# Kernel optimization log

Hardware: AMD Instinct MI355X
Metric: run time of the kernel (lower is better)

Reference implementation:

```python
import jax, jax.numpy as jnp
import numpy as np

NUM_MAX_PATHS = 10
LANE_FEAT_DIM = 128
SEQ_LEN = 80
BATCH = 256

def setup_inputs() -> dict:
    key = jax.random.key(0)
    ks = jax.random.split(key, 8)
    H = LANE_FEAT_DIM
    return {
        "agent_past_motion_context": jax.random.normal(ks[0], (BATCH, 128), dtype=jnp.float32),
        "possible_lanes": jax.random.normal(ks[1], (SEQ_LEN, BATCH * NUM_MAX_PATHS, 2), dtype=jnp.float32),
        "W_emb": jax.random.normal(ks[2], (H, 5), dtype=jnp.float32) * 0.1,
        "b_emb": jax.random.normal(ks[3], (H,), dtype=jnp.float32) * 0.1,
        "W_ih": jax.random.normal(ks[4], (4 * H, H), dtype=jnp.float32) * 0.1,
        "W_hh": jax.random.normal(ks[5], (4 * H, H), dtype=jnp.float32) * 0.1,
        "b_ih": jax.random.normal(ks[6], (4 * H,), dtype=jnp.float32) * 0.1,
        "b_hh": jax.random.normal(ks[7], (4 * H,), dtype=jnp.float32) * 0.1,
    }

def _lane_features(lanes):
    # lanes: [S, BL, 2]. Build 5-dim feature: (x, y, dx, dy, yaw).
    diff = lanes[1:] - lanes[:-1]                        # [S-1, BL, 2]
    diff = jnp.concatenate([jnp.zeros_like(lanes[:1]), diff], axis=0)
    # yaw = atan2(y, x) vs reference vector (1, 0)
    yaw = jnp.arctan2(lanes[..., 1], lanes[..., 0])      # [S, BL]
    ext = jnp.concatenate([lanes, diff, yaw[..., None]], axis=-1)  # [S, BL, 5]
    # lanes containing any NaN produce all-zero features (original conditional)
    valid = jnp.logical_not(jnp.any(jnp.isnan(lanes), axis=(0, 2)))  # [BL]
    return jnp.where(valid[None, :, None], ext, 0.0)

def _lstm(emb, W_ih, W_hh, b_ih, b_hh):
    H = W_hh.shape[1]
    BL = emb.shape[1]
    # precompute input projections for all steps: [S, BL, 4H]
    x_proj = jnp.einsum('sbi,gi->sbg', emb, W_ih) + b_ih

    def step(carry, xg):
        h, c = carry
        gates = xg + h @ W_hh.T + b_hh
        i, f, g, o = jnp.split(gates, 4, axis=-1)
        c = jax.nn.sigmoid(f) * c + jax.nn.sigmoid(i) * jnp.tanh(g)
        h = jax.nn.sigmoid(o) * jnp.tanh(c)
        return (h, c), None

    h0 = jnp.zeros((BL, H), dtype=emb.dtype)
    (h, c), _ = jax.lax.scan(step, (h0, h0), x_proj)
    return h

def reference(agent_past_motion_context, possible_lanes, W_emb, b_emb, W_ih, W_hh, b_ih, b_hh):
    b = agent_past_motion_context.shape[0]
    BL = possible_lanes.shape[1]
    num_max_paths = BL // b
    H = W_emb.shape[0]
    ext = _lane_features(possible_lanes)                         # [S, BL, 5]
    emb = jax.nn.relu(ext @ W_emb.T + b_emb)                     # [S, BL, H]
    h = _lstm(emb, W_ih, W_hh, b_ih, b_hh)                       # [BL, H]
    return h.reshape(b, num_max_paths, H)
```

## Files before the change

kernel.cpp:

```cpp
#include <hip/hip_runtime.h>
#include <stdint.h>

#define S_LEN 80
#define H_DIM 128
#define ROWS 10
#define MROWS 16
#define BLOCK_T 512

#define NL2E  (-1.44269504088896f)
#define N2L2E (-2.88539008177793f)

typedef __bf16 bf16x8 __attribute__((ext_vector_type(8)));
typedef unsigned short u16x8 __attribute__((ext_vector_type(8)));
typedef unsigned short u16x4 __attribute__((ext_vector_type(4)));
typedef float f32x4 __attribute__((ext_vector_type(4)));

__device__ __forceinline__ float sigy(float y) {
    return __builtin_amdgcn_rcpf(1.0f + __builtin_amdgcn_exp2f(y));
}
__device__ __forceinline__ float tanhy(float y) {
    return 2.0f * __builtin_amdgcn_rcpf(1.0f + __builtin_amdgcn_exp2f(y)) - 1.0f;
}
__device__ __forceinline__ unsigned short bfbits(float f) {
    return __builtin_bit_cast(unsigned short, (__bf16)f);
}

#define MFMA16(acc, va, wb) \
    asm("v_mfma_f32_16x16x32_bf16 %0, %1, %2, %0" : "+v"(acc) : "v"(va), "a"(wb))

__global__ __launch_bounds__(BLOCK_T, 2)
void lane_lstm(const float* __restrict__ lanes,
               const float* __restrict__ W_emb, const float* __restrict__ b_emb,
               const float* __restrict__ W_ih,  const float* __restrict__ W_hh,
               const float* __restrict__ b_ih,  const float* __restrict__ b_hh,
               float* __restrict__ out, int BL)
{
    __shared__ __align__(16) float ext_lds[S_LEN * ROWS * 5];
    __shared__ __align__(16) unsigned short emb_lds[2][MROWS * H_DIM];
    __shared__ __align__(16) unsigned short h_lds[2][MROWS * H_DIM];
    __shared__ int valid_lds[MROWS];

    const int t    = threadIdx.x;
    const int lane = t & 63;
    const int wv   = t >> 6;
    const int row0 = blockIdx.x * ROWS;

    if (t < MROWS) valid_lds[t] = 1;
    {
        u16x4 z = {0, 0, 0, 0};
        *(u16x4*)((char*)&h_lds[0][0] + t * 8) = z;
    }
    __syncthreads();

    for (int p = t; p < S_LEN * ROWS; p += BLOCK_T) {
        int s = p / ROWS;
        int r = p - s * ROWS;
        int bl = row0 + r;
        float x = 0.f, y = 0.f, dx = 0.f, dy = 0.f;
        if (bl < BL) {
            const float* lp = lanes + ((size_t)s * BL + bl) * 2;
            x = lp[0]; y = lp[1];
            if (s > 0) {
                const float* lq = lanes + ((size_t)(s - 1) * BL + bl) * 2;
                dx = x - lq[0]; dy = y - lq[1];
            }
            if (__builtin_isnan(x) || __builtin_isnan(y)) valid_lds[r] = 0;
        }
        float* e = &ext_lds[p * 5];
        e[0] = x; e[1] = y; e[2] = dx; e[3] = dy; e[4] = atan2f(y, x);
    }

    const int hcol = wv * 16 + (lane & 15);
    const int kb0  = (lane >> 4) << 3;
    f32x4 wih[4][4], whh[4][4];
    float bia[4];
    #pragma unroll
    for (int g = 0; g < 4; ++g) {
        const float sc = (g == 2) ? N2L2E : NL2E;
        bia[g] = (b_ih[g * H_DIM + hcol] + b_hh[g * H_DIM + hcol]) * sc;
        #pragma unroll
        for (int kt = 0; kt < 4; ++kt) {
            const float* pa = &W_ih[(size_t)(g * H_DIM + hcol) * H_DIM + kt * 32 + kb0];
            const float* pb = &W_hh[(size_t)(g * H_DIM + hcol) * H_DIM + kt * 32 + kb0];
            u16x8 ta, tb;
            #pragma unroll
            for (int j = 0; j < 8; ++j) { ta[j] = bfbits(pa[j] * sc); tb[j] = bfbits(pb[j] * sc); }
            wih[g][kt] = __builtin_bit_cast(f32x4, ta);
            whh[g][kt] = __builtin_bit_cast(f32x4, tb);
        }
    }
    #pragma unroll
    for (int g = 0; g < 4; ++g) {
        #pragma unroll
        for (int kt = 0; kt < 4; ++kt) {
            asm volatile("" : "+a"(wih[g][kt]));
            asm volatile("" : "+a"(whh[g][kt]));
        }
    }

    const int er  = t >> 5;
    const int ec0 = (t & 31) << 2;
    float wemb[4][5], bemb[4];
    #pragma unroll
    for (int j = 0; j < 4; ++j) {
        #pragma unroll
        for (int d = 0; d < 5; ++d) wemb[j][d] = W_emb[(ec0 + j) * 5 + d];
        bemb[j] = b_emb[ec0 + j];
    }
    const int ebyte = ((er << 8) + (ec0 << 1)) ^ ((er & 7) << 4);

    auto emb_store = [&](int s, int b) {
        float x0 = 0.f, x1 = 0.f, x2 = 0.f, x3 = 0.f, x4 = 0.f;
        if (er < ROWS && valid_lds[er] && row0 + er < BL) {
            const float* e = &ext_lds[(s * ROWS + er) * 5];
            x0 = e[0]; x1 = e[1]; x2 = e[2]; x3 = e[3]; x4 = e[4];
        }
        u16x4 ev;
        #pragma unroll
        for (int j = 0; j < 4; ++j) {
            float a = bemb[j];
            a += wemb[j][0] * x0; a += wemb[j][1] * x1; a += wemb[j][2] * x2;
            a += wemb[j][3] * x3; a += wemb[j][4] * x4;
            ev[j] = bfbits(fmaxf(a, 0.f));
        }
        *(u16x4*)((char*)&emb_lds[b][0] + ebyte) = ev;
    };

    const int arow  = lane & 15;
    const int akey  = (arow & 7) << 4;
    const int abase = (arow << 8) + ((lane >> 4) << 4);
    const int crow  = (lane >> 4) << 2;

    __syncthreads();
    emb_store(0, 0);
    __syncthreads();

    f32x4 xp0 = {bia[0], bia[0], bia[0], bia[0]};
    f32x4 xp1 = {bia[1], bia[1], bia[1], bia[1]};
    f32x4 xp2 = {bia[2], bia[2], bia[2], bia[2]};
    f32x4 xp3 = {bia[3], bia[3], bia[3], bia[3]};
    {
        const char* eb = (const char*)&emb_lds[0][0];
        #pragma unroll
        for (int kt = 0; kt < 4; ++kt) {
            bf16x8 ae = *(const bf16x8*)(eb + ((abase + kt * 64) ^ akey));
            MFMA16(xp0, ae, wih[0][kt]);
            MFMA16(xp1, ae, wih[1][kt]);
            MFMA16(xp2, ae, wih[2][kt]);
            MFMA16(xp3, ae, wih[3][kt]);
        }
    }
    emb_store(1, 1);
    __syncthreads();

    float c0 = 0.f, c1 = 0.f, c2 = 0.f, c3 = 0.f;

    for (int s = 0; s < S_LEN; ++s) {
        const char* hb = (const char*)&h_lds[s & 1][0];
        const char* en = (const char*)&emb_lds[(s + 1) & 1][0];

        bf16x8 ah0 = *(const bf16x8*)(hb + ((abase + 0 * 64) ^ akey));
        bf16x8 ah1 = *(const bf16x8*)(hb + ((abase + 1 * 64) ^ akey));
        bf16x8 ah2 = *(const bf16x8*)(hb + ((abase + 2 * 64) ^ akey));
        bf16x8 ah3 = *(const bf16x8*)(hb + ((abase + 3 * 64) ^ akey));
        f32x4 g0 = xp0, g1 = xp1, g2 = xp2, g3 = xp3;
        MFMA16(g0, ah0, whh[0][0]); MFMA16(g1, ah0, whh[1][0]);
        MFMA16(g2, ah0, whh[2][0]); MFMA16(g3, ah0, whh[3][0]);
        MFMA16(g0, ah1, whh[0][1]); MFMA16(g1, ah1, whh[1][1]);
        MFMA16(g2, ah1, whh[2][1]); MFMA16(g3, ah1, whh[3][1]);
        MFMA16(g0, ah2, whh[0][2]); MFMA16(g1, ah2, whh[1][2]);
        MFMA16(g2, ah2, whh[2][2]); MFMA16(g3, ah2, whh[3][2]);
        MFMA16(g0, ah3, whh[0][3]); MFMA16(g1, ah3, whh[1][3]);
        MFMA16(g2, ah3, whh[2][3]); MFMA16(g3, ah3, whh[3][3]);

        if (s + 1 < S_LEN) {
            bf16x8 ae0 = *(const bf16x8*)(en + ((abase + 0 * 64) ^ akey));
            bf16x8 ae1 = *(const bf16x8*)(en + ((abase + 1 * 64) ^ akey));
            bf16x8 ae2 = *(const bf16x8*)(en + ((abase + 2 * 64) ^ akey));
            bf16x8 ae3 = *(const bf16x8*)(en + ((abase + 3 * 64) ^ akey));
            xp0 = (f32x4){bia[0], bia[0], bia[0], bia[0]};
            xp1 = (f32x4){bia[1], bia[1], bia[1], bia[1]};
            xp2 = (f32x4){bia[2], bia[2], bia[2], bia[2]};
            xp3 = (f32x4){bia[3], bia[3], bia[3], bia[3]};
            MFMA16(xp0, ae0, wih[0][0]); MFMA16(xp1, ae0, wih[1][0]);
            MFMA16(xp2, ae0, wih[2][0]); MFMA16(xp3, ae0, wih[3][0]);
            MFMA16(xp0, ae1, wih[0][1]); MFMA16(xp1, ae1, wih[1][1]);
            MFMA16(xp2, ae1, wih[2][1]); MFMA16(xp3, ae1, wih[3][1]);
            MFMA16(xp0, ae2, wih[0][2]); MFMA16(xp1, ae2, wih[1][2]);
            MFMA16(xp2, ae2, wih[2][2]); MFMA16(xp3, ae2, wih[3][2]);
            MFMA16(xp0, ae3, wih[0][3]); MFMA16(xp1, ae3, wih[1][3]);
            MFMA16(xp2, ae3, wih[2][3]); MFMA16(xp3, ae3, wih[3][3]);
            if (s + 2 < S_LEN) emb_store(s + 2, s & 1);
        }

        char* hn = (char*)&h_lds[(s + 1) & 1][0];
        float hv0, hv1, hv2, hv3;
        c0 = sigy(g1[0]) * c0 + sigy(g0[0]) * tanhy(g2[0]);  hv0 = sigy(g3[0]) * tanhy(c0 * N2L2E);
        c1 = sigy(g1[1]) * c1 + sigy(g0[1]) * tanhy(g2[1]);  hv1 = sigy(g3[1]) * tanhy(c1 * N2L2E);
        c2 = sigy(g1[2]) * c2 + sigy(g0[2]) * tanhy(g2[2]);  hv2 = sigy(g3[2]) * tanhy(c2 * N2L2E);
        c3 = sigy(g1[3]) * c3 + sigy(g0[3]) * tanhy(g2[3]);  hv3 = sigy(g3[3]) * tanhy(c3 * N2L2E);

        #pragma unroll
        for (int i = 0; i < 4; ++i) {
            const float hvi = (i == 0) ? hv0 : (i == 1) ? hv1 : (i == 2) ? hv2 : hv3;
            const int r = crow + i;
            const int byte = ((r << 8) + (hcol << 1)) ^ ((r & 7) << 4);
            *(unsigned short*)(hn + byte) = bfbits(hvi);
        }

        if (s == S_LEN - 1) {
            #pragma unroll
            for (int i = 0; i < 4; ++i) {
                const float hvi = (i == 0) ? hv0 : (i == 1) ? hv1 : (i == 2) ? hv2 : hv3;
                const int r = crow + i;
                if (r < ROWS && row0 + r < BL)
                    out[(size_t)(row0 + r) * H_DIM + hcol] = hvi;
            }
        }
        __syncthreads();
    }
}

extern "C" void kernel_launch(void* const* d_in, const int* in_sizes, int n_in,
                              void* d_out, int out_size, void* d_ws, size_t ws_size,
                              hipStream_t stream) {
    const float* lanes = (const float*)d_in[1];
    const float* W_emb = (const float*)d_in[2];
    const float* b_emb = (const float*)d_in[3];
    const float* W_ih  = (const float*)d_in[4];
    const float* W_hh  = (const float*)d_in[5];
    const float* b_ih  = (const float*)d_in[6];
    const float* b_hh  = (const float*)d_in[7];
    float* out = (float*)d_out;

    const int BL   = in_sizes[1] / (2 * S_LEN);
    const int grid = (BL + ROWS - 1) / ROWS;

    lane_lstm<<<dim3(grid), dim3(BLOCK_T), 0, stream>>>(
        lanes, W_emb, b_emb, W_ih, W_hh, b_ih, b_hh, out, BL);
}
```

Measured before the change: 116.7 us.

## Split waves into input-projection producers and recurrent consumers via LDS

The eight waves are split into two roles. Four waves compute the input projection for the next step from the embeddings and write it to a double-buffered LDS area. The other four waves consume those projections, run the recurrent MFMAs and gate math, and each covers 32 hidden columns instead of 16. The goal is to take the input-projection MFMAs off the recurrent critical path and overlap them with the gate work. In exchange it adds LDS traffic for the projections, doubles the register weight footprint per wave for each matrix, and switches the inline-asm MFMA to the compiler builtin.

Measured after the change: 198.7 us. 1.7x slower.

```diff
diff --git a/kernel.cpp b/kernel.cpp
--- a/kernel.cpp
+++ b/kernel.cpp
@@ -25,8 +25,8 @@
     return __builtin_bit_cast(unsigned short, (__bf16)f);
 }
 
-#define MFMA16(acc, va, wb) \
-    asm("v_mfma_f32_16x16x32_bf16 %0, %1, %2, %0" : "+v"(acc) : "v"(va), "a"(wb))
+#define MFMA(A, B, C) __builtin_amdgcn_mfma_f32_16x16x32_bf16((A), (B), (C), 0, 0, 0)
+#define WB(W) __builtin_bit_cast(bf16x8, W)
 
 __global__ __launch_bounds__(BLOCK_T, 2)
 void lane_lstm(const float* __restrict__ lanes,
@@ -38,11 +38,14 @@
     __shared__ __align__(16) float ext_lds[S_LEN * ROWS * 5];
     __shared__ __align__(16) unsigned short emb_lds[2][MROWS * H_DIM];
     __shared__ __align__(16) unsigned short h_lds[2][MROWS * H_DIM];
+    __shared__ __align__(16) float xp_lds[2 * 32 * 64 * 4];
     __shared__ int valid_lds[MROWS];
 
     const int t    = threadIdx.x;
     const int lane = t & 63;
     const int wv   = t >> 6;
+    const int role = wv >> 2;
+    const int q    = wv & 3;
     const int row0 = blockIdx.x * ROWS;
 
     if (t < MROWS) valid_lds[t] = 1;
@@ -70,35 +73,36 @@
         e[0] = x; e[1] = y; e[2] = dx; e[3] = dy; e[4] = atan2f(y, x);
     }
 
-    const int hcol = wv * 16 + (lane & 15);
-    const int kb0  = (lane >> 4) << 3;
-    f32x4 wih[4][4], whh[4][4];
-    float bia[4];
+    const float* Wsrc = role ? W_hh : W_ih;
+    const int kb0 = (lane >> 4) << 3;
+    f32x4 wgt[4][2][4];
+    float bsc[4][2];
     #pragma unroll
     for (int g = 0; g < 4; ++g) {
         const float sc = (g == 2) ? N2L2E : NL2E;
-        bia[g] = (b_ih[g * H_DIM + hcol] + b_hh[g * H_DIM + hcol]) * sc;
-        #pragma unroll
-        for (int kt = 0; kt < 4; ++kt) {
-            const float* pa = &W_ih[(size_t)(g * H_DIM + hcol) * H_DIM + kt * 32 + kb0];
-            const float* pb = &W_hh[(size_t)(g * H_DIM + hcol) * H_DIM + kt * 32 + kb0];
-            u16x8 ta, tb;
-            #pragma unroll
-            for (int j = 0; j < 8; ++j) { ta[j] = bfbits(pa[j] * sc); tb[j] = bfbits(pb[j] * sc); }
-            wih[g][kt] = __builtin_bit_cast(f32x4, ta);
-            whh[g][kt] = __builtin_bit_cast(f32x4, tb);
+        #pragma unroll
+        for (int nt = 0; nt < 2; ++nt) {
+            const int col = g * H_DIM + q * 32 + nt * 16 + (lane & 15);
+            bsc[g][nt] = (b_ih[col] + b_hh[col]) * sc;
+            #pragma unroll
+            for (int kt = 0; kt < 4; ++kt) {
+                const float* pw = Wsrc + (size_t)col * H_DIM + kt * 32 + kb0;
+                u16x8 tw;
+                #pragma unroll
+                for (int j = 0; j < 8; ++j) tw[j] = bfbits(pw[j] * sc);
+                wgt[g][nt][kt] = __builtin_bit_cast(f32x4, tw);
+            }
         }
     }
     #pragma unroll
-    for (int g = 0; g < 4; ++g) {
-        #pragma unroll
-        for (int kt = 0; kt < 4; ++kt) {
-            asm volatile("" : "+a"(wih[g][kt]));
-            asm volatile("" : "+a"(whh[g][kt]));
-        }
-    }
-
-    const int er  = t >> 5;
+    for (int g = 0; g < 4; ++g)
+        #pragma unroll
+        for (int nt = 0; nt < 2; ++nt)
+            #pragma unroll
+            for (int kt = 0; kt < 4; ++kt)
+                asm volatile("" : "+a"(wgt[g][nt][kt]));
+
+    const int er2 = (t >> 5) & 7;
     const int ec0 = (t & 31) << 2;
     float wemb[4][5], bemb[4];
     #pragma unroll
@@ -107,117 +111,164 @@
         for (int d = 0; d < 5; ++d) wemb[j][d] = W_emb[(ec0 + j) * 5 + d];
         bemb[j] = b_emb[ec0 + j];
     }
-    const int ebyte = ((er << 8) + (ec0 << 1)) ^ ((er & 7) << 4);
-
-    auto emb_store = [&](int s, int b) {
-        float x0 = 0.f, x1 = 0.f, x2 = 0.f, x3 = 0.f, x4 = 0.f;
-        if (er < ROWS && valid_lds[er] && row0 + er < BL) {
-            const float* e = &ext_lds[(s * ROWS + er) * 5];
-            x0 = e[0]; x1 = e[1]; x2 = e[2]; x3 = e[3]; x4 = e[4];
-        }
-        u16x4 ev;
-        #pragma unroll
-        for (int j = 0; j < 4; ++j) {
-            float a = bemb[j];
-            a += wemb[j][0] * x0; a += wemb[j][1] * x1; a += wemb[j][2] * x2;
-            a += wemb[j][3] * x3; a += wemb[j][4] * x4;
-            ev[j] = bfbits(fmaxf(a, 0.f));
-        }
-        *(u16x4*)((char*)&emb_lds[b][0] + ebyte) = ev;
+
+    auto emb_store = [&](int sx, int b) {
+        #pragma unroll
+        for (int rr = 0; rr < 2; ++rr) {
+            const int r = er2 + rr * 8;
+            float x0 = 0.f, x1 = 0.f, x2 = 0.f, x3 = 0.f, x4 = 0.f;
+            if (r < ROWS && valid_lds[r] && row0 + r < BL) {
+                const float* e = &ext_lds[(sx * ROWS + r) * 5];
+                x0 = e[0]; x1 = e[1]; x2 = e[2]; x3 = e[3]; x4 = e[4];
+            }
+            u16x4 ev;
+            #pragma unroll
+            for (int j = 0; j < 4; ++j) {
+                float a = bemb[j];
+                a += wemb[j][0] * x0; a += wemb[j][1] * x1; a += wemb[j][2] * x2;
+                a += wemb[j][3] * x3; a += wemb[j][4] * x4;
+                ev[j] = bfbits(fmaxf(a, 0.f));
+            }
+            const int byte = ((r << 8) + (ec0 << 1)) ^ ((r & 7) << 4);
+            *(u16x4*)((char*)&emb_lds[b][0] + byte) = ev;
+        }
     };
 
     const int arow  = lane & 15;
     const int akey  = (arow & 7) << 4;
     const int abase = (arow << 8) + ((lane >> 4) << 4);
     const int crow  = (lane >> 4) << 2;
-
-    __syncthreads();
-    emb_store(0, 0);
-    __syncthreads();
-
-    f32x4 xp0 = {bia[0], bia[0], bia[0], bia[0]};
-    f32x4 xp1 = {bia[1], bia[1], bia[1], bia[1]};
-    f32x4 xp2 = {bia[2], bia[2], bia[2], bia[2]};
-    f32x4 xp3 = {bia[3], bia[3], bia[3], bia[3]};
-    {
+    const int xpbase = q * 8192 + lane * 16;
+
+    __syncthreads();
+    if (!role) emb_store(0, 0);
+    __syncthreads();
+    if (!role) {
         const char* eb = (const char*)&emb_lds[0][0];
-        #pragma unroll
-        for (int kt = 0; kt < 4; ++kt) {
-            bf16x8 ae = *(const bf16x8*)(eb + ((abase + kt * 64) ^ akey));
-            MFMA16(xp0, ae, wih[0][kt]);
-            MFMA16(xp1, ae, wih[1][kt]);
-            MFMA16(xp2, ae, wih[2][kt]);
-            MFMA16(xp3, ae, wih[3][kt]);
-        }
-    }
-    emb_store(1, 1);
-    __syncthreads();
-
-    float c0 = 0.f, c1 = 0.f, c2 = 0.f, c3 = 0.f;
-
-    for (int s = 0; s < S_LEN; ++s) {
+        bf16x8 ae0 = *(const bf16x8*)(eb + ((abase + 0 * 64) ^ akey));
+        bf16x8 ae1 = *(const bf16x8*)(eb + ((abase + 1 * 64) ^ akey));
+        bf16x8 ae2 = *(const bf16x8*)(eb + ((abase + 2 * 64) ^ akey));
+        bf16x8 ae3 = *(const bf16x8*)(eb + ((abase + 3 * 64) ^ akey));
+        #pragma unroll
+        for (int g = 0; g < 4; ++g) {
+            #pragma unroll
+            for (int nt = 0; nt < 2; ++nt) {
+                f32x4 a;
+                a[0] = bsc[g][nt]; a[1] = bsc[g][nt]; a[2] = bsc[g][nt]; a[3] = bsc[g][nt];
+                a = MFMA(ae0, WB(wgt[g][nt][0]), a);
+                a = MFMA(ae1, WB(wgt[g][nt][1]), a);
+                a = MFMA(ae2, WB(wgt[g][nt][2]), a);
+                a = MFMA(ae3, WB(wgt[g][nt][3]), a);
+                *(f32x4*)((char*)&xp_lds[0] + xpbase + (g * 2 + nt) * 1024) = a;
+            }
+        }
+        emb_store(1, 1);
+    }
+    __syncthreads();
+
+    float c[2][4] = {{0.f, 0.f, 0.f, 0.f}, {0.f, 0.f, 0.f, 0.f}};
+
+    for (int s = 0; s < S_LEN - 1; ++s) {
+        if (!role) {
+            const char* en = (const char*)&emb_lds[(s + 1) & 1][0];
+            bf16x8 ae0 = *(const bf16x8*)(en + ((abase + 0 * 64) ^ akey));
+            bf16x8 ae1 = *(const bf16x8*)(en + ((abase + 1 * 64) ^ akey));
+            bf16x8 ae2 = *(const bf16x8*)(en + ((abase + 2 * 64) ^ akey));
+            bf16x8 ae3 = *(const bf16x8*)(en + ((abase + 3 * 64) ^ akey));
+            char* xw = (char*)&xp_lds[0] + ((s + 1) & 1) * 32768 + xpbase;
+            #pragma unroll
+            for (int g = 0; g < 4; ++g) {
+                #pragma unroll
+                for (int nt = 0; nt < 2; ++nt) {
+                    f32x4 a;
+                    a[0] = bsc[g][nt]; a[1] = bsc[g][nt]; a[2] = bsc[g][nt]; a[3] = bsc[g][nt];
+                    a = MFMA(ae0, WB(wgt[g][nt][0]), a);
+                    a = MFMA(ae1, WB(wgt[g][nt][1]), a);
+                    a = MFMA(ae2, WB(wgt[g][nt][2]), a);
+                    a = MFMA(ae3, WB(wgt[g][nt][3]), a);
+                    *(f32x4*)(xw + (g * 2 + nt) * 1024) = a;
+                }
+            }
+            if (s + 2 < S_LEN) emb_store(s + 2, s & 1);
+        } else {
+            const char* hb = (const char*)&h_lds[s & 1][0];
+            const char* xr = (const char*)&xp_lds[0] + (s & 1) * 32768 + xpbase;
+            bf16x8 ah0 = *(const bf16x8*)(hb + ((abase + 0 * 64) ^ akey));
+            bf16x8 ah1 = *(const bf16x8*)(hb + ((abase + 1 * 64) ^ akey));
+            bf16x8 ah2 = *(const bf16x8*)(hb + ((abase + 2 * 64) ^ akey));
+            bf16x8 ah3 = *(const bf16x8*)(hb + ((abase + 3 * 64) ^ akey));
+            f32x4 ga[4][2];
+            #pragma unroll
+            for (int g = 0; g < 4; ++g)
+                #pragma unroll
+                for (int nt = 0; nt < 2; ++nt)
+                    ga[g][nt] = *(const f32x4*)(xr + (g * 2 + nt) * 1024);
+            #pragma unroll
+            for (int g = 0; g < 4; ++g) {
+                #pragma unroll
+                for (int nt = 0; nt < 2; ++nt) {
+                    ga[g][nt] = MFMA(ah0, WB(wgt[g][nt][0]), ga[g][nt]);
+                    ga[g][nt] = MFMA(ah1, WB(wgt[g][nt][1]), ga[g][nt]);
+                    ga[g][nt] = MFMA(ah2, WB(wgt[g][nt][2]), ga[g][nt]);
+                    ga[g][nt] = MFMA(ah3, WB(wgt[g][nt][3]), ga[g][nt]);
+                }
+            }
+            char* hn = (char*)&h_lds[(s + 1) & 1][0];
+            #pragma unroll
+            for (int nt = 0; nt < 2; ++nt) {
+                #pragma unroll
+                for (int i = 0; i < 4; ++i) {
+                    float cc = sigy(ga[1][nt][i]) * c[nt][i]
+                             + sigy(ga[0][nt][i]) * tanhy(ga[2][nt][i]);
+                    c[nt][i] = cc;
+                    const float hv = sigy(ga[3][nt][i]) * tanhy(cc * N2L2E);
+                    const int r  = crow + i;
+                    const int hc = q * 32 + nt * 16 + (lane & 15);
+                    const int byte = ((r << 8) + (hc << 1)) ^ ((r & 7) << 4);
+                    *(unsigned short*)(hn + byte) = bfbits(hv);
+                }
+            }
+        }
+        __syncthreads();
+    }
+
+    if (role) {
+        const int s = S_LEN - 1;
         const char* hb = (const char*)&h_lds[s & 1][0];
-        const char* en = (const char*)&emb_lds[(s + 1) & 1][0];
-
+        const char* xr = (const char*)&xp_lds[0] + (s & 1) * 32768 + xpbase;
         bf16x8 ah0 = *(const bf16x8*)(hb + ((abase + 0 * 64) ^ akey));
         bf16x8 ah1 = *(const bf16x8*)(hb + ((abase + 1 * 64) ^ akey));
         bf16x8 ah2 = *(const bf16x8*)(hb + ((abase + 2 * 64) ^ akey));
         bf16x8 ah3 = *(const bf16x8*)(hb + ((abase + 3 * 64) ^ akey));
-        f32x4 g0 = xp0, g1 = xp1, g2 = xp2, g3 = xp3;
-        MFMA16(g0, ah0, whh[0][0]); MFMA16(g1, ah0, whh[1][0]);
-        MFMA16(g2, ah0, whh[2][0]); MFMA16(g3, ah0, whh[3][0]);
-        MFMA16(g0, ah1, whh[0][1]); MFMA16(g1, ah1, whh[1][1]);
-        MFMA16(g2, ah1, whh[2][1]); MFMA16(g3, ah1, whh[3][1]);
-        MFMA16(g0, ah2, whh[0][2]); MFMA16(g1, ah2, whh[1][2]);
-        MFMA16(g2, ah2, whh[2][2]); MFMA16(g3, ah2, whh[3][2]);
-        MFMA16(g0, ah3, whh[0][3]); MFMA16(g1, ah3, whh[1][3]);
-        MFMA16(g2, ah3, whh[2][3]); MFMA16(g3, ah3, whh[3][3]);
-
-        if (s + 1 < S_LEN) {
-            bf16x8 ae0 = *(const bf16x8*)(en + ((abase + 0 * 64) ^ akey));
-            bf16x8 ae1 = *(const bf16x8*)(en + ((abase + 1 * 64) ^ akey));
-            bf16x8 ae2 = *(const bf16x8*)(en + ((abase + 2 * 64) ^ akey));
-            bf16x8 ae3 = *(const bf16x8*)(en + ((abase + 3 * 64) ^ akey));
-            xp0 = (f32x4){bia[0], bia[0], bia[0], bia[0]};
-            xp1 = (f32x4){bia[1], bia[1], bia[1], bia[1]};
-            xp2 = (f32x4){bia[2], bia[2], bia[2], bia[2]};
-            xp3 = (f32x4){bia[3], bia[3], bia[3], bia[3]};
-            MFMA16(xp0, ae0, wih[0][0]); MFMA16(xp1, ae0, wih[1][0]);
-            MFMA16(xp2, ae0, wih[2][0]); MFMA16(xp3, ae0, wih[3][0]);
-            MFMA16(xp0, ae1, wih[0][1]); MFMA16(xp1, ae1, wih[1][1]);
-            MFMA16(xp2, ae1, wih[2][1]); MFMA16(xp3, ae1, wih[3][1]);
-            MFMA16(xp0, ae2, wih[0][2]); MFMA16(xp1, ae2, wih[1][2]);
-            MFMA16(xp2, ae2, wih[2][2]); MFMA16(xp3, ae2, wih[3][2]);
-            MFMA16(xp0, ae3, wih[0][3]); MFMA16(xp1, ae3, wih[1][3]);
-            MFMA16(xp2, ae3, wih[2][3]); MFMA16(xp3, ae3, wih[3][3]);
-            if (s + 2 < S_LEN) emb_store(s + 2, s & 1);
-        }
-
-        char* hn = (char*)&h_lds[(s + 1) & 1][0];
-        float hv0, hv1, hv2, hv3;
-        c0 = sigy(g1[0]) * c0 + sigy(g0[0]) * tanhy(g2[0]);  hv0 = sigy(g3[0]) * tanhy(c0 * N2L2E);
-        c1 = sigy(g1[1]) * c1 + sigy(g0[1]) * tanhy(g2[1]);  hv1 = sigy(g3[1]) * tanhy(c1 * N2L2E);
-        c2 = sigy(g1[2]) * c2 + sigy(g0[2]) * tanhy(g2[2]);  hv2 = sigy(g3[2]) * tanhy(c2 * N2L2E);
-        c3 = sigy(g1[3]) * c3 + sigy(g0[3]) * tanhy(g2[3]);  hv3 = sigy(g3[3]) * tanhy(c3 * N2L2E);
-
-        #pragma unroll
-        for (int i = 0; i < 4; ++i) {
-            const float hvi = (i == 0) ? hv0 : (i == 1) ? hv1 : (i == 2) ? hv2 : hv3;
-            const int r = crow + i;
-            const int byte = ((r << 8) + (hcol << 1)) ^ ((r & 7) << 4);
-            *(unsigned short*)(hn + byte) = bfbits(hvi);
-        }
-
-        if (s == S_LEN - 1) {
+        f32x4 ga[4][2];
+        #pragma unroll
+        for (int g = 0; g < 4; ++g)
+            #pragma unroll
+            for (int nt = 0; nt < 2; ++nt)
+                ga[g][nt] = *(const f32x4*)(xr + (g * 2 + nt) * 1024);
+        #pragma unroll
+        for (int g = 0; g < 4; ++g) {
+            #pragma unroll
+            for (int nt = 0; nt < 2; ++nt) {
+                ga[g][nt] = MFMA(ah0, WB(wgt[g][nt][0]), ga[g][nt]);
+                ga[g][nt] = MFMA(ah1, WB(wgt[g][nt][1]), ga[g][nt]);
+                ga[g][nt] = MFMA(ah2, WB(wgt[g][nt][2]), ga[g][nt]);
+                ga[g][nt] = MFMA(ah3, WB(wgt[g][nt][3]), ga[g][nt]);
+            }
+        }
+        #pragma unroll
+        for (int nt = 0; nt < 2; ++nt) {
             #pragma unroll
             for (int i = 0; i < 4; ++i) {
-                const float hvi = (i == 0) ? hv0 : (i == 1) ? hv1 : (i == 2) ? hv2 : hv3;
-                const int r = crow + i;
+                float cc = sigy(ga[1][nt][i]) * c[nt][i]
+                         + sigy(ga[0][nt][i]) * tanhy(ga[2][nt][i]);
+                const float hv = sigy(ga[3][nt][i]) * tanhy(cc * N2L2E);
+                const int r  = crow + i;
+                const int hc = q * 32 + nt * 16 + (lane & 15);
                 if (r < ROWS && row0 + r < BL)
-                    out[(size_t)(row0 + r) * H_DIM + hcol] = hvi;
-            }
-        }
-        __syncthreads();
+                    out[(size_t)(row0 + r) * H_DIM + hc] = hv;
+            }
+        }
     }
 }
 
```
